# Optimization experiments

Measured on AMD Instinct MI355X. Metric: run time of the kernel, lower is better.

The kernel has to match this reference:

```python
import jax, jax.numpy as jnp
import numpy as np

B, L, N, F, H, HOR = 32, 12, 1024, 2, 128, 12


def setup_inputs() -> dict:
    key = jax.random.key(0)
    ks = jax.random.split(key, 9)
    x = jax.random.normal(ks[0], (B, L, N, F), dtype=jnp.float32)
    # A_phys: sparse-ish binary physical adjacency, then normalize_adj: add self-loops, row-normalize
    A_phys = (jax.random.uniform(ks[1], (N, N)) < 0.05).astype(jnp.float32)
    A = A_phys + jnp.eye(N, dtype=jnp.float32)
    A = A / (A.sum(axis=1, keepdims=True) + 1e-6)
    # GraphGRUCell params (single layer): lin_x: F -> 3H, lin_h: H -> 3H
    sx = 1.0 / np.sqrt(F)
    sh = 1.0 / np.sqrt(H)
    W_x = jax.random.uniform(ks[2], (F, 3 * H), minval=-sx, maxval=sx)
    b_x = jax.random.uniform(ks[3], (3 * H,), minval=-sx, maxval=sx)
    W_h = jax.random.uniform(ks[4], (H, 3 * H), minval=-sh, maxval=sh)
    b_h = jax.random.uniform(ks[5], (3 * H,), minval=-sh, maxval=sh)
    # head: H -> horizon
    W_head = jax.random.uniform(ks[6], (H, HOR), minval=-sh, maxval=sh)
    b_head = jax.random.uniform(ks[7], (HOR,), minval=-sh, maxval=sh)
    return {"x": x, "A": A, "W_x": W_x, "b_x": b_x, "W_h": W_h, "b_h": b_h,
            "W_head": W_head, "b_head": b_head}


def reference(x, A, W_x, b_x, W_h, b_h, W_head, b_head):
    Bv, Lv, Nv, Fv = x.shape
    Hv = W_h.shape[0]

    def step(h, xt):
        # graph aggregation of hidden state: [N,N] x [B,N,H] -> [B,N,H]
        Ah = jnp.einsum('ij,bjh->bih', A, h)
        x_gates = xt @ W_x + b_x          # [B,N,3H]
        h_gates = Ah @ W_h + b_h          # [B,N,3H]
        z_x, r_x, n_x = jnp.split(x_gates, 3, axis=-1)
        z_h, r_h, n_h = jnp.split(h_gates, 3, axis=-1)
        z = jax.nn.sigmoid(z_x + z_h)
        r = jax.nn.sigmoid(r_x + r_h)
        n = jnp.tanh(n_x + r * n_h)
        h_new = (1.0 - z) * n + z * h
        return h_new, None

    h0 = jnp.zeros((Bv, Nv, Hv), dtype=x.dtype)
    xs = jnp.moveaxis(x, 1, 0)  # [L,B,N,F]
    h, _ = jax.lax.scan(step, h0, xs)
    y = (h @ W_head + b_head).transpose(0, 2, 1)  # [B, horizon, N]
    return y
```

## Files before the change

kernel.cpp:

```cpp
#include <hip/hip_runtime.h>
#include <hip/hip_bf16.h>

#define BB 32
#define LL 12
#define NN 1024
#define HH 128
#define HORN 12
#define G3 384

typedef unsigned short u16;
typedef unsigned int u32;
typedef unsigned long long u64;
typedef __attribute__((ext_vector_type(8))) short short8;
typedef __attribute__((ext_vector_type(4))) float f32x4;

__device__ __forceinline__ u16 to_bf16(float f) {
    return __builtin_bit_cast(u16, __float2bfloat16(f));
}
__device__ __forceinline__ float bf_to_f(u32 bits) {
    return __builtin_bit_cast(float, bits << 16);
}
__device__ __forceinline__ void gl16(const u16* g, char* l) {
    __builtin_amdgcn_global_load_lds((const __attribute__((address_space(1))) u32*)g,
                                     (__attribute__((address_space(3))) u32*)l, 16, 0, 0);
}

__global__ void prep_abf(const float* __restrict__ A, u16* __restrict__ Abf) {
    int t = blockIdx.x * blockDim.x + threadIdx.x;
    float4 v = ((const float4*)A)[t];
    ushort4 o;
    o.x = to_bf16(v.x); o.y = to_bf16(v.y); o.z = to_bf16(v.z); o.w = to_bf16(v.w);
    ((ushort4*)Abf)[t] = o;
}

__global__ void prep_whT(const float* __restrict__ W_h, u16* __restrict__ whT) {
    int t = blockIdx.x * blockDim.x + threadIdx.x;
    if (t >= HH * G3) return;
    int c = t / HH, k = t % HH;
    whT[c * HH + k] = to_bf16(W_h[k * G3 + c]);
}

template <bool FIRST>
__global__ __launch_bounds__(256, 2) void gru_step(
    const u16* __restrict__ Abf, const u16* __restrict__ hT_old,
    u16* __restrict__ hT_new, const u16* __restrict__ whT,
    const float* __restrict__ x, const float* __restrict__ W_x,
    const float* __restrict__ b_x, const float* __restrict__ b_h, int t) {
    __shared__ __align__(16) char smem[65536];

    int bid = blockIdx.x;
    int swz = (bid & 7) * 64 + (bid >> 3);
    int b = swz >> 4;
    int i0 = (swz & 15) * 64;
    int tid = threadIdx.x;
    int w = tid >> 6, lane = tid & 63;
    int lcol = lane & 15, kgrp = lane >> 4;
    int wm = w >> 1, wn = w & 1;
    u32 swzl = (u32)((lcol & 7) << 4);

    u32 a_b = (u32)((wm * 32 + lcol) * 128);
    u32 b_b = (u32)(8192 + (wn * 64 + lcol) * 128);

    f32x4 acc[2][4];
#pragma unroll
    for (int m = 0; m < 2; ++m)
#pragma unroll
        for (int n = 0; n < 4; ++n) acc[m][n] = (f32x4){0.f, 0.f, 0.f, 0.f};

    if (!FIRST) {
        int lr3 = lane >> 3, lc8 = lane & 7;
        const u16* ag[2]; u32 al[2];
        const u16* bg[4]; u32 bl[4];
#pragma unroll
        for (int q = 0; q < 2; ++q) {
            int r = w * 16 + q * 8 + lr3;
            ag[q] = Abf + (size_t)(i0 + r) * 1024 + (lc8 ^ (r & 7)) * 8;
            al[q] = (u32)(w * 2048 + q * 1024);
        }
#pragma unroll
        for (int q = 0; q < 4; ++q) {
            int r = w * 32 + q * 8 + lr3;
            bg[q] = hT_old + (size_t)b * 131072 + (size_t)r * 1024 + (lc8 ^ (r & 7)) * 8;
            bl[q] = (u32)(8192 + w * 4096 + q * 1024);
        }

#pragma unroll
        for (int q = 0; q < 2; ++q) gl16(ag[q], smem + al[q]);
#pragma unroll
        for (int q = 0; q < 4; ++q) gl16(bg[q], smem + bl[q]);
        __syncthreads();

        for (int c = 0; c < 16; ++c) {
            u32 sb = (u32)((c & 1) * 24576);
            if (c < 15) {
                int o = (c + 1) * 64;
                u32 db = (u32)(((c + 1) & 1) * 24576);
#pragma unroll
                for (int q = 0; q < 2; ++q) gl16(ag[q] + o, smem + db + al[q]);
#pragma unroll
                for (int q = 0; q < 4; ++q) gl16(bg[q] + o, smem + db + bl[q]);
            }
#pragma unroll
            for (int ks = 0; ks < 2; ++ks) {
                u32 kb = ((u32)(ks * 64 + kgrp * 16)) ^ swzl;
                short8 a0 = *(const short8*)(smem + sb + a_b + kb);
                short8 a1 = *(const short8*)(smem + sb + a_b + 2048 + kb);
                short8 b0 = *(const short8*)(smem + sb + b_b + kb);
                short8 b1 = *(const short8*)(smem + sb + b_b + 2048 + kb);
                short8 b2 = *(const short8*)(smem + sb + b_b + 4096 + kb);
                short8 b3 = *(const short8*)(smem + sb + b_b + 6144 + kb);
                acc[0][0] = __builtin_amdgcn_mfma_f32_16x16x32_bf16(a0, b0, acc[0][0], 0, 0, 0);
                acc[0][1] = __builtin_amdgcn_mfma_f32_16x16x32_bf16(a0, b1, acc[0][1], 0, 0, 0);
                acc[0][2] = __builtin_amdgcn_mfma_f32_16x16x32_bf16(a0, b2, acc[0][2], 0, 0, 0);
                acc[0][3] = __builtin_amdgcn_mfma_f32_16x16x32_bf16(a0, b3, acc[0][3], 0, 0, 0);
                acc[1][0] = __builtin_amdgcn_mfma_f32_16x16x32_bf16(a1, b0, acc[1][0], 0, 0, 0);
                acc[1][1] = __builtin_amdgcn_mfma_f32_16x16x32_bf16(a1, b1, acc[1][1], 0, 0, 0);
                acc[1][2] = __builtin_amdgcn_mfma_f32_16x16x32_bf16(a1, b2, acc[1][2], 0, 0, 0);
                acc[1][3] = __builtin_amdgcn_mfma_f32_16x16x32_bf16(a1, b3, acc[1][3], 0, 0, 0);
            }
            __syncthreads();
        }
    }

#pragma unroll
    for (int m = 0; m < 2; ++m)
#pragma unroll
        for (int n = 0; n < 4; ++n)
#pragma unroll
            for (int ri = 0; ri < 4; ++ri) {
                int row = wm * 32 + m * 16 + kgrp * 4 + ri;
                int col = wn * 64 + n * 16 + lcol;
                *(u16*)(smem + 49152 + row * 256 + (((u32)(2 * col)) ^ ((u32)(row & 7) << 4))) =
                    to_bf16(acc[m][n][ri]);
            }
    __syncthreads();

#pragma unroll
    for (int sub = 0; sub < 2; ++sub) {
        int hh = w * 32 + sub * 16 + lcol;
        short8 bw[3][4];
#pragma unroll
        for (int g = 0; g < 3; ++g)
#pragma unroll
            for (int ks = 0; ks < 4; ++ks)
                bw[g][ks] = *(const short8*)(whT + (size_t)(g * 128 + hh) * 128 + ks * 32 + kgrp * 8);

        f32x4 acc2[4][3];
#pragma unroll
        for (int rt = 0; rt < 4; ++rt)
#pragma unroll
            for (int g = 0; g < 3; ++g) acc2[rt][g] = (f32x4){0.f, 0.f, 0.f, 0.f};

#pragma unroll
        for (int rt = 0; rt < 4; ++rt) {
            u32 ab2 = (u32)(49152 + (rt * 16 + lcol) * 256);
#pragma unroll
            for (int ks = 0; ks < 4; ++ks) {
                short8 a2 = *(const short8*)(smem + ab2 + (((u32)(ks * 64 + kgrp * 16)) ^ swzl));
                acc2[rt][0] = __builtin_amdgcn_mfma_f32_16x16x32_bf16(a2, bw[0][ks], acc2[rt][0], 0, 0, 0);
                acc2[rt][1] = __builtin_amdgcn_mfma_f32_16x16x32_bf16(a2, bw[1][ks], acc2[rt][1], 0, 0, 0);
                acc2[rt][2] = __builtin_amdgcn_mfma_f32_16x16x32_bf16(a2, bw[2][ks], acc2[rt][2], 0, 0, 0);
            }
        }

        float bxz = b_x[hh], bxr = b_x[128 + hh], bxn = b_x[256 + hh];
        float bhz = b_h[hh], bhr = b_h[128 + hh], bhn = b_h[256 + hh];
        float wx0z = W_x[hh], wx0r = W_x[128 + hh], wx0n = W_x[256 + hh];
        float wx1z = W_x[G3 + hh], wx1r = W_x[G3 + 128 + hh], wx1n = W_x[G3 + 256 + hh];
        const u16* hrow = hT_old + (size_t)b * 131072 + (size_t)hh * 1024 + i0;
#pragma unroll
        for (int rt = 0; rt < 4; ++rt) {
            u64 h4 = 0;
            if (!FIRST) h4 = *(const u64*)(hrow + rt * 16 + kgrp * 4);
#pragma unroll
            for (int ri = 0; ri < 4; ++ri) {
                int rl = rt * 16 + kgrp * 4 + ri;
                int i = i0 + rl;
                const float* xp = x + ((size_t)(b * LL + t) * NN + i) * 2;
                float x0 = xp[0], x1 = xp[1];
                float zin = acc2[rt][0][ri] + bhz + fmaf(x0, wx0z, fmaf(x1, wx1z, bxz));
                float rin = acc2[rt][1][ri] + bhr + fmaf(x0, wx0r, fmaf(x1, wx1r, bxr));
                float z = 1.f / (1.f + __expf(-zin));
                float rg = 1.f / (1.f + __expf(-rin));
                float nin = fmaf(rg, acc2[rt][2][ri] + bhn, fmaf(x0, wx0n, fmaf(x1, wx1n, bxn)));
                nin = fmaxf(nin, -40.f);
                float e = __expf(-2.f * nin);
                float n = (1.f - e) / (1.f + e);
                float hold = bf_to_f((u32)((h4 >> (16 * ri)) & 0xffffu));
                float hv = fmaf(z, hold - n, n);
                *(u16*)(smem + hh * 128 + (((u32)(2 * rl)) ^ ((u32)(hh & 7) << 4))) = to_bf16(hv);
            }
        }
    }
    __syncthreads();
#pragma unroll
    for (int c2 = 0; c2 < 4; ++c2) {
        int o = c2 * 4096 + tid * 16;
        int nr = o >> 7, cb = o & 127;
        uint4 v = *(const uint4*)(smem + nr * 128 + (((u32)cb) ^ ((u32)(nr & 7) << 4)));
        *(uint4*)((char*)(hT_new + (size_t)b * 131072 + (size_t)nr * 1024 + i0) + cb) = v;
    }
}

__global__ __launch_bounds__(256) void head_kernel(
    const u16* __restrict__ hT, const float* __restrict__ W_head,
    const float* __restrict__ b_head, float* __restrict__ out) {
    __shared__ float wl[HH * HORN];
    __shared__ float bl[HORN];
    int tid = threadIdx.x;
    for (int ix = tid; ix < HH * HORN; ix += 256) wl[ix] = W_head[ix];
    if (tid < HORN) bl[tid] = b_head[tid];
    __syncthreads();
    int blk = blockIdx.x;
    int b = blk >> 2;
    int i = (blk & 3) * 256 + tid;
    const u16* hp = hT + (size_t)b * 131072 + i;
    float acc[HORN];
#pragma unroll
    for (int hor = 0; hor < HORN; ++hor) acc[hor] = bl[hor];
    for (int hh = 0; hh < HH; ++hh) {
        float hv = bf_to_f((u32)hp[hh * 1024]);
#pragma unroll
        for (int hor = 0; hor < HORN; ++hor)
            acc[hor] = fmaf(hv, wl[hh * HORN + hor], acc[hor]);
    }
#pragma unroll
    for (int hor = 0; hor < HORN; ++hor)
        out[((size_t)b * HORN + hor) * NN + i] = acc[hor];
}

extern "C" void kernel_launch(void* const* d_in, const int* in_sizes, int n_in,
                              void* d_out, int out_size, void* d_ws, size_t ws_size,
                              hipStream_t stream) {
    const float* x = (const float*)d_in[0];
    const float* A = (const float*)d_in[1];
    const float* W_x = (const float*)d_in[2];
    const float* b_x = (const float*)d_in[3];
    const float* W_h = (const float*)d_in[4];
    const float* b_h = (const float*)d_in[5];
    const float* W_head = (const float*)d_in[6];
    const float* b_head = (const float*)d_in[7];
    float* out = (float*)d_out;
    char* ws = (char*)d_ws;

    u16* hT0 = (u16*)(ws + 0);
    u16* hT1 = (u16*)(ws + 8388608);
    u16* Abf = (u16*)(ws + 16777216);
    u16* whT = (u16*)(ws + 18874368);

    prep_abf<<<1024, 256, 0, stream>>>(A, Abf);
    prep_whT<<<(HH * G3 + 255) / 256, 256, 0, stream>>>(W_h, whT);

    gru_step<true><<<512, 256, 0, stream>>>(Abf, hT1, hT0, whT, x, W_x, b_x, b_h, 0);
    u16* hTo = hT0; u16* hTn = hT1;
    for (int t = 1; t < LL; ++t) {
        gru_step<false><<<512, 256, 0, stream>>>(Abf, hTo, hTn, whT, x, W_x, b_x, b_h, t);
        u16* tmp = hTo; hTo = hTn; hTn = tmp;
    }
    head_kernel<<<BB * 4, 256, 0, stream>>>(hTo, W_head, b_head, out);
}
```

Measured before the change: 324.6 us.

## Deepen GEMM prefetch pipeline, reuse staged h tile, and raise MFMA priority

```diff
diff --git a/kernel.cpp b/kernel.cpp
--- a/kernel.cpp
+++ b/kernel.cpp
@@ -67,6 +67,8 @@
 #pragma unroll
         for (int n = 0; n < 4; ++n) acc[m][n] = (f32x4){0.f, 0.f, 0.f, 0.f};
 
+    u64 hreg[2][4] = {};
+
     if (!FIRST) {
         int lr3 = lane >> 3, lc8 = lane & 7;
         const u16* ag[2]; u32 al[2];
@@ -88,18 +90,34 @@
         for (int q = 0; q < 2; ++q) gl16(ag[q], smem + al[q]);
 #pragma unroll
         for (int q = 0; q < 4; ++q) gl16(bg[q], smem + bl[q]);
-        __syncthreads();
-
+#pragma unroll
+        for (int q = 0; q < 2; ++q) gl16(ag[q] + 64, smem + 24576 + al[q]);
+#pragma unroll
+        for (int q = 0; q < 4; ++q) gl16(bg[q] + 64, smem + 24576 + bl[q]);
+
+        int cstar = i0 >> 6;
         for (int c = 0; c < 16; ++c) {
             u32 sb = (u32)((c & 1) * 24576);
-            if (c < 15) {
-                int o = (c + 1) * 64;
-                u32 db = (u32)(((c + 1) & 1) * 24576);
-#pragma unroll
-                for (int q = 0; q < 2; ++q) gl16(ag[q] + o, smem + db + al[q]);
-#pragma unroll
-                for (int q = 0; q < 4; ++q) gl16(bg[q] + o, smem + db + bl[q]);
-            }
+            if (c < 15) asm volatile("s_waitcnt vmcnt(6)" ::: "memory");
+            else        asm volatile("s_waitcnt vmcnt(0)" ::: "memory");
+            __builtin_amdgcn_s_barrier();
+            __builtin_amdgcn_sched_barrier(0);
+
+            if (c == cstar) {
+#pragma unroll
+                for (int sub = 0; sub < 2; ++sub) {
+                    int hh = w * 32 + sub * 16 + lcol;
+                    u32 rb = sb + 8192u + (u32)(hh * 128);
+                    u32 sw = (u32)((hh & 7) << 4);
+#pragma unroll
+                    for (int rt = 0; rt < 4; ++rt)
+                        hreg[sub][rt] = *(const u64*)(smem + rb + (((u32)(rt * 32 + kgrp * 8)) ^ sw));
+                }
+                asm volatile("s_waitcnt lgkmcnt(0)" ::: "memory");
+                __builtin_amdgcn_sched_barrier(0);
+            }
+
+            __builtin_amdgcn_s_setprio(1);
 #pragma unroll
             for (int ks = 0; ks < 2; ++ks) {
                 u32 kb = ((u32)(ks * 64 + kgrp * 16)) ^ swzl;
@@ -118,8 +136,19 @@
                 acc[1][2] = __builtin_amdgcn_mfma_f32_16x16x32_bf16(a1, b2, acc[1][2], 0, 0, 0);
                 acc[1][3] = __builtin_amdgcn_mfma_f32_16x16x32_bf16(a1, b3, acc[1][3], 0, 0, 0);
             }
-            __syncthreads();
-        }
+            __builtin_amdgcn_s_setprio(0);
+            asm volatile("" ::: "memory");
+            __builtin_amdgcn_s_barrier();
+            if (c < 14) {
+                int o = (c + 2) * 64;
+#pragma unroll
+                for (int q = 0; q < 2; ++q) gl16(ag[q] + o, smem + sb + al[q]);
+#pragma unroll
+                for (int q = 0; q < 4; ++q) gl16(bg[q] + o, smem + sb + bl[q]);
+            }
+        }
+        asm volatile("" ::: "memory");
+        __builtin_amdgcn_s_barrier();
     }
 
 #pragma unroll
@@ -151,6 +180,7 @@
 #pragma unroll
             for (int g = 0; g < 3; ++g) acc2[rt][g] = (f32x4){0.f, 0.f, 0.f, 0.f};
 
+        __builtin_amdgcn_s_setprio(1);
 #pragma unroll
         for (int rt = 0; rt < 4; ++rt) {
             u32 ab2 = (u32)(49152 + (rt * 16 + lcol) * 256);
@@ -162,16 +192,15 @@
                 acc2[rt][2] = __builtin_amdgcn_mfma_f32_16x16x32_bf16(a2, bw[2][ks], acc2[rt][2], 0, 0, 0);
             }
         }
+        __builtin_amdgcn_s_setprio(0);
 
         float bxz = b_x[hh], bxr = b_x[128 + hh], bxn = b_x[256 + hh];
         float bhz = b_h[hh], bhr = b_h[128 + hh], bhn = b_h[256 + hh];
         float wx0z = W_x[hh], wx0r = W_x[128 + hh], wx0n = W_x[256 + hh];
         float wx1z = W_x[G3 + hh], wx1r = W_x[G3 + 128 + hh], wx1n = W_x[G3 + 256 + hh];
-        const u16* hrow = hT_old + (size_t)b * 131072 + (size_t)hh * 1024 + i0;
 #pragma unroll
         for (int rt = 0; rt < 4; ++rt) {
-            u64 h4 = 0;
-            if (!FIRST) h4 = *(const u64*)(hrow + rt * 16 + kgrp * 4);
+            u64 h4 = hreg[sub][rt];
 #pragma unroll
             for (int ri = 0; ri < 4; ++ri) {
                 int rl = rt * 16 + kgrp * 4 + ri;
```

New measurement: 306.3 us. 5.6% less time.
